# Kernel optimization log

Measured on AMD Instinct MI355X. Metric: run time of the kernel, lower is better.

Reference implementation:

```python
import jax, jax.numpy as jnp
import numpy as np

BLANK = 0  # matches __init__ default blank=0
T, V = 1048576, 128

def setup_inputs() -> dict:
    key = jax.random.key(0)
    emission = jax.random.normal(key, (T, V), dtype=jnp.float32)
    return {"emission": emission}

def reference(emission):
    # Greedy CTC decode, array form (strings are not jit-expressible).
    # idx[t] = argmax over labels at step t
    idx = jnp.argmax(emission, axis=-1).astype(jnp.int32)          # [T]
    # Run-length dedup: keep a step if its symbol differs from the previous one
    prev = jnp.concatenate([jnp.full((1,), -1, idx.dtype), idx[:-1]])
    keep = (idx != prev) & (idx != BLANK)                          # [T] bool, emitted symbols
    # Max logit per step, zeroed at non-kept steps (float view of the decode path)
    max_logit = jnp.max(emission, axis=-1)                         # [T]
    path_score = jnp.where(keep, max_logit, jnp.zeros((), emission.dtype))
    return idx, keep, path_score
```

## Files before the change

### kernel.cpp

```cpp
#include <hip/hip_runtime.h>


#define VLAB 128

__global__ void ctc_pass1(const float* __restrict__ em,
                          int* __restrict__ idx_ws,
                          float* __restrict__ max_ws,
                          float* __restrict__ out_idx,
                          int T) {
    int t = blockIdx.x * blockDim.x + threadIdx.x;
    if (t >= T) return;
    const float4* row = reinterpret_cast<const float4*>(em) + (size_t)t * (VLAB / 4);
    float best = -3.402823466e38f;
    int bidx = 0;
    #pragma unroll
    for (int k = 0; k < VLAB / 4; ++k) {
        float4 v = row[k];
        if (v.x > best) { best = v.x; bidx = 4 * k + 0; }
        if (v.y > best) { best = v.y; bidx = 4 * k + 1; }
        if (v.z > best) { best = v.z; bidx = 4 * k + 2; }
        if (v.w > best) { best = v.w; bidx = 4 * k + 3; }
    }
    idx_ws[t] = bidx;
    max_ws[t] = best;
    out_idx[t] = (float)bidx;
}

__global__ void ctc_pass2(const int* __restrict__ idx_ws,
                          const float* __restrict__ max_ws,
                          float* __restrict__ out_keep,
                          float* __restrict__ out_score,
                          int T) {
    int t = blockIdx.x * blockDim.x + threadIdx.x;
    if (t >= T) return;
    int cur = idx_ws[t];
    int prev = (t == 0) ? -1 : idx_ws[t - 1];
    bool keep = (cur != prev) && (cur != 0);
    out_keep[t]  = keep ? 1.0f : 0.0f;
    out_score[t] = keep ? max_ws[t] : 0.0f;
}

extern "C" void kernel_launch(void* const* d_in, const int* in_sizes, int n_in,
                              void* d_out, int out_size, void* d_ws, size_t ws_size,
                              hipStream_t stream) {
    const float* em = (const float*)d_in[0];
    const int T = in_sizes[0] / VLAB;

    float* out       = (float*)d_out;
    float* out_idx   = out;
    float* out_keep  = out + (size_t)T;
    float* out_score = out + (size_t)2 * T;

    int*   idx_ws = (int*)d_ws;
    float* max_ws = (float*)((char*)d_ws + (size_t)T * sizeof(int));

    const int block = 256;
    const int grid = (T + block - 1) / block;
    ctc_pass1<<<grid, block, 0, stream>>>(em, idx_ws, max_ws, out_idx, T);
    ctc_pass2<<<grid, block, 0, stream>>>(idx_ws, max_ws, out_keep, out_score, T);
}
```

Measured before the change: 695.4 us.

## Fuse argmax and dedup into one kernel with coalesced half-wave row reduction

Replaces the two-pass design with one kernel. Each half-wave of 32 lanes reads one 512-byte row as float4s, so the loads are coalesced, and reduces the argmax with xor shuffles. Per-row results go to shared memory, and the previous row's index at the block boundary is recomputed. This removes the strided per-thread row reads, the workspace round trip and the second launch. In exchange it adds shuffle reduction work and assumes T is a multiple of 256.

```diff
diff --git a/kernel.cpp b/kernel.cpp
--- a/kernel.cpp
+++ b/kernel.cpp
@@ -2,42 +2,86 @@
 
 
 #define VLAB 128
+#define ROWS_PER_BLOCK 256
 
-__global__ void ctc_pass1(const float* __restrict__ em,
-                          int* __restrict__ idx_ws,
-                          float* __restrict__ max_ws,
-                          float* __restrict__ out_idx,
-                          int T) {
-    int t = blockIdx.x * blockDim.x + threadIdx.x;
-    if (t >= T) return;
-    const float4* row = reinterpret_cast<const float4*>(em) + (size_t)t * (VLAB / 4);
-    float best = -3.402823466e38f;
-    int bidx = 0;
-    #pragma unroll
-    for (int k = 0; k < VLAB / 4; ++k) {
-        float4 v = row[k];
-        if (v.x > best) { best = v.x; bidx = 4 * k + 0; }
-        if (v.y > best) { best = v.y; bidx = 4 * k + 1; }
-        if (v.z > best) { best = v.z; bidx = 4 * k + 2; }
-        if (v.w > best) { best = v.w; bidx = 4 * k + 3; }
-    }
-    idx_ws[t] = bidx;
-    max_ws[t] = best;
-    out_idx[t] = (float)bidx;
+__device__ __forceinline__ void argmax4(const float4 v, int l, float& best, int& idx) {
+    best = v.x; idx = l * 4;
+    if (v.y > best) { best = v.y; idx = l * 4 + 1; }
+    if (v.z > best) { best = v.z; idx = l * 4 + 2; }
+    if (v.w > best) { best = v.w; idx = l * 4 + 3; }
 }
 
-__global__ void ctc_pass2(const int* __restrict__ idx_ws,
-                          const float* __restrict__ max_ws,
-                          float* __restrict__ out_keep,
-                          float* __restrict__ out_score,
-                          int T) {
-    int t = blockIdx.x * blockDim.x + threadIdx.x;
-    if (t >= T) return;
-    int cur = idx_ws[t];
-    int prev = (t == 0) ? -1 : idx_ws[t - 1];
-    bool keep = (cur != prev) && (cur != 0);
-    out_keep[t]  = keep ? 1.0f : 0.0f;
-    out_score[t] = keep ? max_ws[t] : 0.0f;
+__global__ __launch_bounds__(256) void ctc_fused(const float4* __restrict__ em4,
+                                                 float* __restrict__ out_idx,
+                                                 float* __restrict__ out_keep,
+                                                 float* __restrict__ out_score) {
+    __shared__ int   s_idx[ROWS_PER_BLOCK + 1];
+    __shared__ float s_max[ROWS_PER_BLOCK + 1];
+
+    const int tid  = threadIdx.x;
+    const int wave = tid >> 6;
+    const int lane = tid & 63;
+    const int half = lane >> 5;
+    const int l    = lane & 31;
+    const int base = blockIdx.x * ROWS_PER_BLOCK;
+
+    #pragma unroll
+    for (int i = 0; i < 8; ++i) {
+        const int r0 = base + i * 32 + wave * 8;
+        float4 v4[4];
+        #pragma unroll
+        for (int j = 0; j < 4; ++j) {
+            v4[j] = em4[(size_t)(r0 + 2 * j) * 32 + lane];
+        }
+        float bv[4]; int bi[4];
+        #pragma unroll
+        for (int j = 0; j < 4; ++j) argmax4(v4[j], l, bv[j], bi[j]);
+
+        #pragma unroll
+        for (int m = 16; m >= 1; m >>= 1) {
+            #pragma unroll
+            for (int j = 0; j < 4; ++j) {
+                float ov = __shfl_xor(bv[j], m, 32);
+                int   oi = __shfl_xor(bi[j], m, 32);
+                if (ov > bv[j] || (ov == bv[j] && oi < bi[j])) { bv[j] = ov; bi[j] = oi; }
+            }
+        }
+        if (l == 0) {
+            #pragma unroll
+            for (int j = 0; j < 4; ++j) {
+                int slot = (r0 - base) + 2 * j + half + 1;
+                s_idx[slot] = bi[j];
+                s_max[slot] = bv[j];
+            }
+        }
+    }
+
+    if (wave == 0) {
+        if (blockIdx.x > 0) {
+            float4 v = em4[(size_t)(base - 1) * 32 + lane];
+            float best; int idx;
+            argmax4(v, l, best, idx);
+            #pragma unroll
+            for (int m = 16; m >= 1; m >>= 1) {
+                float ov = __shfl_xor(best, m, 32);
+                int   oi = __shfl_xor(idx, m, 32);
+                if (ov > best || (ov == best && oi < idx)) { best = ov; idx = oi; }
+            }
+            if (lane == 0) s_idx[0] = idx;
+        } else if (tid == 0) {
+            s_idx[0] = -1;
+        }
+    }
+
+    __syncthreads();
+
+    const int r   = base + tid;
+    const int cur = s_idx[tid + 1];
+    const int prv = s_idx[tid];
+    const bool keep = (cur != prv) && (cur != 0);
+    out_idx[r]   = (float)cur;
+    out_keep[r]  = keep ? 1.0f : 0.0f;
+    out_score[r] = keep ? s_max[tid + 1] : 0.0f;
 }
 
 extern "C" void kernel_launch(void* const* d_in, const int* in_sizes, int n_in,
@@ -51,11 +95,7 @@
     float* out_keep  = out + (size_t)T;
     float* out_score = out + (size_t)2 * T;
 
-    int*   idx_ws = (int*)d_ws;
-    float* max_ws = (float*)((char*)d_ws + (size_t)T * sizeof(int));
-
-    const int block = 256;
-    const int grid = (T + block - 1) / block;
-    ctc_pass1<<<grid, block, 0, stream>>>(em, idx_ws, max_ws, out_idx, T);
-    ctc_pass2<<<grid, block, 0, stream>>>(idx_ws, max_ws, out_keep, out_score, T);
+    const int grid = T / ROWS_PER_BLOCK;
+    ctc_fused<<<grid, ROWS_PER_BLOCK, 0, stream>>>(
+        reinterpret_cast<const float4*>(em), out_idx, out_keep, out_score);
 }
```

Result: no change. 685.1 us (-1.5%).
